# Performance work log

Hardware: AMD Instinct MI355X
Metric: run time of the kernel (lower is better)

Reference implementation:

```python
import jax, jax.numpy as jnp
import numpy as np

LN_EPS = 1e-5


def setup_inputs() -> dict:
    key = jax.random.key(0)
    ks = jax.random.split(key, 6)
    B, N, C, H = 8, 4096, 768, 12
    D = C // H
    x = jax.random.normal(ks[0], (B, N, C), dtype=jnp.float32)
    w_qkv = jax.random.normal(ks[1], (3 * C, C), dtype=jnp.float32) * (C ** -0.5)
    w_proj = jax.random.normal(ks[2], (C, C), dtype=jnp.float32) * (C ** -0.5)
    b_proj = jnp.zeros((C,), dtype=jnp.float32)
    # trunc_normal_(std=0.02) approximated by clipped normal
    p1 = jnp.clip(jax.random.normal(ks[3], (H, N), dtype=jnp.float32) * 0.02, -0.04, 0.04)
    p2 = jnp.clip(jax.random.normal(ks[4], (H, N), dtype=jnp.float32) * 0.02, -0.04, 0.04)
    gamma = jnp.ones((D,), dtype=jnp.float32)
    beta = jnp.zeros((D,), dtype=jnp.float32)
    return {"x": x, "w_qkv": w_qkv, "w_proj": w_proj, "b_proj": b_proj,
            "p1": p1, "p2": p2, "gamma": gamma, "beta": beta}


def _layernorm(h, gamma, beta):
    mu = jnp.mean(h, axis=-1, keepdims=True)
    var = jnp.var(h, axis=-1, keepdims=True)
    return (h - mu) * jax.lax.rsqrt(var + LN_EPS) * gamma + beta


def reference(x, w_qkv, w_proj, b_proj, p1, p2, gamma, beta):
    B, N, C = x.shape
    H = p1.shape[0]
    D = C // H
    # qkv projection (no bias): [B,N,3C] -> [3,B,H,N,D]
    qkv = (x @ w_qkv.T).reshape(B, N, 3, H, D).transpose(2, 0, 3, 1, 4)
    q, k, v = qkv[0], qkv[1], qkv[2]
    # weighted k*v reduction over sequence: [B,H,D]
    modulator = jnp.einsum('hn,bhnd->bhd', p2, k * v)
    modulator = _layernorm(modulator, gamma, beta)
    # broadcast modulation back over N: [B,H,N,D]
    modulator = jnp.einsum('hn,bhd->bhnd', p1, modulator)
    out = (q * modulator).transpose(0, 2, 1, 3).reshape(B, N, C)
    return out @ w_proj.T + b_proj
```

## Files before the change

kernel.cpp:

```cpp
#include <hip/hip_runtime.h>
#include <stdint.h>
#include <stddef.h>

#define LN_EPS 1e-5f

typedef __bf16 bf16;
typedef __bf16 bf16x8 __attribute__((ext_vector_type(8)));
typedef __bf16 bf16x4 __attribute__((ext_vector_type(4)));
typedef float f32x4 __attribute__((ext_vector_type(4)));

#define GL16(gp, lp)                                                                   \
  __builtin_amdgcn_global_load_lds((__attribute__((address_space(1))) uint32_t*)(gp),  \
                                   (__attribute__((address_space(3))) uint32_t*)(lp),  \
                                   16, 0, 0)

#define SBAR   asm volatile("s_barrier" ::: "memory")
#define VMW(N) asm volatile("s_waitcnt vmcnt(" #N ")" ::: "memory")
#define LGK(N) asm volatile("s_waitcnt lgkmcnt(" #N ")" ::: "memory")
#define NOWAIT ((void)0)

#define XV4   6291456
#define WQV4  442368
#define WPV4  147456
__global__ __launch_bounds__(256) void cvt_all(const float* __restrict__ x,
                                               const float* __restrict__ wq,
                                               const float* __restrict__ wp,
                                               bf16* __restrict__ xb,
                                               bf16* __restrict__ wqb,
                                               bf16* __restrict__ wpb) {
  int i = blockIdx.x * 256 + threadIdx.x;
  const float* src; bf16* dst; int off;
  if (i < XV4)              { src = x;  dst = xb;  off = i; }
  else if (i < XV4 + WQV4)  { src = wq; dst = wqb; off = i - XV4; }
  else                      { src = wp; dst = wpb; off = i - (XV4 + WQV4); }
  const float4 v = ((const float4*)src)[off];
  bf16x4 o;
  o[0] = (bf16)v.x; o[1] = (bf16)v.y; o[2] = (bf16)v.z; o[3] = (bf16)v.w;
  ((bf16x4*)dst)[off] = o;
}

#define STAGE_A2(H, SL) do {                          \
    GL16(pA0 + (H)*32, dA + (SL)*8192);               \
    GL16(pA1 + (H)*32, dA + (SL)*8192 + 4096); } while (0)

#define STAGE_B2(H, SL) do {                          \
    GL16(pB0 + (H)*32, dB + (SL)*8192);               \
    GL16(pB1 + (H)*32, dB + (SL)*8192 + 4096); } while (0)

#define RD_B(DST, SL)                                                              \
    _Pragma("unroll") for (int n = 0; n < 4; ++n)                                  \
      DST[n] = *(const bf16x8*)(ldsB + (SL)*8192 + (rB + n*16)*32 + colE)

#define RD_A0(DST, SL)                                                             \
    _Pragma("unroll") for (int m = 0; m < 4; ++m)                                  \
      DST[m] = *(const bf16x8*)(ldsA + (SL)*8192 + (rA + m*16)*32 + colE)

#define RD_A1(SL)                                                                  \
    _Pragma("unroll") for (int m = 0; m < 4; ++m)                                  \
      af1[m] = *(const bf16x8*)(ldsA + (SL)*8192 + (rA + 64 + m*16)*32 + colE)

#define MM(AF, BF, MO)                                                             \
    _Pragma("unroll") for (int m = 0; m < 4; ++m)                                  \
      _Pragma("unroll") for (int n = 0; n < 4; ++n)                                \
        acc[(MO) + m][n] = __builtin_amdgcn_mfma_f32_16x16x32_bf16(                \
            AF[m], BF[n], acc[(MO) + m][n], 0, 0, 0)

#define EV_PHASE(SL, A0C, BFC, STG, WAITV) do {       \
    RD_A1(SL);                                        \
    STG;                                              \
    LGK(4);                                           \
    __builtin_amdgcn_sched_barrier(0);                \
    __builtin_amdgcn_s_setprio(1);                    \
    MM(A0C, BFC, 0);                                  \
    __builtin_amdgcn_s_setprio(0);                    \
    WAITV;                                            \
    SBAR;                                             \
  } while (0)

#define OD_PHASE(NSL, A0N, BFN, BFC, STG, LGKW) do {  \
    RD_B(BFN, NSL);                                   \
    RD_A0(A0N, NSL);                                  \
    STG;                                              \
    LGKW;                                             \
    __builtin_amdgcn_sched_barrier(0);                \
    __builtin_amdgcn_s_setprio(1);                    \
    MM(af1, BFC, 4);                                  \
    __builtin_amdgcn_s_setprio(0);                    \
    SBAR;                                             \
  } while (0)

__device__ __forceinline__ void gemm256(const bf16* pA0, const bf16* pA1,
                                        const bf16* pB0, const bf16* pB1,
                                        bf16* sh, f32x4 acc[8][4]) {
  const int tid  = threadIdx.x;
  const int lane = tid & 63;
  const int wave = tid >> 6;
  const int wm   = wave >> 2;
  const int wn   = wave & 3;
  const int l16  = lane & 15;
  const int colE = ((((lane >> 4) * 16) ^ (((l16 >> 1) & 3) << 4)) >> 1);
  bf16* const ldsA = sh;
  bf16* const ldsB = sh + 32768;
  bf16* const dA   = ldsA + tid * 8;
  bf16* const dB   = ldsB + tid * 8;
  const int rA = wm * 128 + l16;
  const int rB = wn * 64 + l16;
  bf16x8 af0X[4], af0Y[4], af1[4], bfX[4], bfY[4];

  STAGE_A2(0, 0); STAGE_B2(0, 0);
  STAGE_A2(1, 1); STAGE_B2(1, 1);
  STAGE_A2(2, 2); STAGE_B2(2, 2);
  VMW(8);
  SBAR;
  RD_B(bfX, 0);
  RD_A0(af0X, 0);

  for (int h4 = 0; h4 < 20; h4 += 4) {
    EV_PHASE(0, af0X, bfX, STAGE_A2(h4 + 3, 3), VMW(6));
    OD_PHASE(1, af0Y, bfY, bfX, STAGE_B2(h4 + 3, 3), LGK(8));
    EV_PHASE(1, af0Y, bfY, STAGE_A2(h4 + 4, 0), VMW(6));
    OD_PHASE(2, af0X, bfX, bfY, STAGE_B2(h4 + 4, 0), LGK(8));
    EV_PHASE(2, af0X, bfX, STAGE_A2(h4 + 5, 1), VMW(6));
    OD_PHASE(3, af0Y, bfY, bfX, STAGE_B2(h4 + 5, 1), LGK(8));
    EV_PHASE(3, af0Y, bfY, STAGE_A2(h4 + 6, 2), VMW(6));
    OD_PHASE(0, af0X, bfX, bfY, STAGE_B2(h4 + 6, 2), LGK(8));
  }
  EV_PHASE(0, af0X, bfX, STAGE_A2(23, 3), VMW(6));
  OD_PHASE(1, af0Y, bfY, bfX, STAGE_B2(23, 3), LGK(8));
  EV_PHASE(1, af0Y, bfY, NOWAIT, VMW(4));
  OD_PHASE(2, af0X, bfX, bfY, NOWAIT, LGK(8));
  EV_PHASE(2, af0X, bfX, NOWAIT, VMW(0));
  OD_PHASE(3, af0Y, bfY, bfX, NOWAIT, LGK(8));
  EV_PHASE(3, af0Y, bfY, NOWAIT, NOWAIT);
  LGK(0);
  __builtin_amdgcn_sched_barrier(0);
  __builtin_amdgcn_s_setprio(1);
  MM(af1, bfY, 4);
  __builtin_amdgcn_s_setprio(0);
  asm volatile("s_waitcnt vmcnt(0) lgkmcnt(0)" ::: "memory");
  __syncthreads();
}

__global__ __launch_bounds__(512, 2) void kv_gemm_reduce(const bf16* __restrict__ A,
                                                         const bf16* __restrict__ B,
                                                         const float* __restrict__ p2,
                                                         float* __restrict__ partials) {
  __shared__ __align__(16) bf16 sh[256 * 264];
  __shared__ float red[4][2][64];

  int lin = blockIdx.y * 6 + blockIdx.x;
  lin = (lin & 7) * 96 + (lin >> 3);
  const int hh   = lin % 6;
  const int mblk = lin / 6;
  const int m0   = mblk * 256;
  const int h0   = hh * 2;

  const int tid = threadIdx.x;
  const int rr  = tid >> 2;
  const int ck  = ((tid & 3) ^ ((tid >> 3) & 3)) * 8;
  const bf16* pA0 = A + (size_t)(m0 + rr) * 768 + ck;
  const bf16* pA1 = pA0 + (size_t)128 * 768;
  const int r1 = 128 + rr;
  const int wr0 = 768 + (((rr >> 6) & 1) * 768) + (h0 + (rr >> 7)) * 64 + (rr & 63);
  const int wr1 = 768 + (((r1 >> 6) & 1) * 768) + (h0 + (r1 >> 7)) * 64 + (r1 & 63);
  const bf16* pB0 = B + (size_t)wr0 * 768 + ck;
  const bf16* pB1 = B + (size_t)wr1 * 768 + ck;

  f32x4 acc[8][4] = {};
  gemm256(pA0, pA1, pB0, pB1, sh, acc);

  const int lane = tid & 63, wave = tid >> 6;
  const int wm = wave >> 2, wn = wave & 3, l16 = lane & 15;
  const int c0 = wn * 64 + l16;
  const int r0 = wm * 128 + (lane >> 4) * 4;
#pragma unroll
  for (int ni = 0; ni < 4; ++ni)
#pragma unroll
    for (int mi = 0; mi < 8; ++mi) {
      bf16x4 pk;
      pk[0] = (bf16)acc[mi][ni][0]; pk[1] = (bf16)acc[mi][ni][1];
      pk[2] = (bf16)acc[mi][ni][2]; pk[3] = (bf16)acc[mi][ni][3];
      *(bf16x4*)(sh + (size_t)(c0 + ni * 16) * 264 + r0 + mi * 16) = pk;
    }
  __syncthreads();

  const int nq = tid >> 7, hl = (tid >> 6) & 1, d = tid & 63;
  const float* pw = p2 + (size_t)(h0 + hl) * 4096 + (m0 & 4095) + nq * 64;
  const bf16* pk = sh + (size_t)(hl * 128 + d) * 264 + nq * 64;
  const bf16* pv = sh + (size_t)(hl * 128 + 64 + d) * 264 + nq * 64;
  float s = 0.f;
#pragma unroll
  for (int nb = 0; nb < 8; ++nb) {
    const bf16x8 k8 = *(const bf16x8*)(pk + nb * 8);
    const bf16x8 v8 = *(const bf16x8*)(pv + nb * 8);
#pragma unroll
    for (int e = 0; e < 8; ++e)
      s += pw[nb * 8 + e] * (float)k8[e] * (float)v8[e];
  }
  red[nq][hl][d] = s;
  __syncthreads();
  if (tid < 128) {
    const int hx = tid >> 6, dd = tid & 63;
    partials[((size_t)mblk * 12 + h0 + hx) * 64 + dd] =
        red[0][hx][dd] + red[1][hx][dd] + red[2][hx][dd] + red[3][hx][dd];
  }
}

__global__ __launch_bounds__(64) void mod_reduce_ln(const float* __restrict__ partials,
                                                    const float* __restrict__ gamma,
                                                    const float* __restrict__ beta,
                                                    float* __restrict__ mod) {
  const int h = blockIdx.x, b = blockIdx.y;
  const int d = threadIdx.x;

  const float* p = partials + ((size_t)(b * 16) * 12 + h) * 64 + d;
  float s = 0.f;
#pragma unroll
  for (int mb = 0; mb < 16; ++mb) s += p[(size_t)mb * 12 * 64];

  float sum = s, sumsq = s * s;
#pragma unroll
  for (int o = 32; o > 0; o >>= 1) {
    sum   += __shfl_xor(sum, o);
    sumsq += __shfl_xor(sumsq, o);
  }
  const float mu  = sum * (1.f / 64.f);
  const float var = sumsq * (1.f / 64.f) - mu * mu;
  const float r   = rsqrtf(var + LN_EPS);
  mod[(b * 12 + h) * 64 + d] = (s - mu) * r * gamma[d] + beta[d];
}

__global__ __launch_bounds__(512, 2) void q_gemm_mod(const bf16* __restrict__ A,
                                                     const bf16* __restrict__ B,
                                                     const float* __restrict__ p1,
                                                     const float* __restrict__ mod,
                                                     bf16* __restrict__ amod) {
  __shared__ __align__(16) bf16 sh[65536];

  int lin = blockIdx.y * 3 + blockIdx.x;
  lin = (lin & 7) * 48 + (lin >> 3);
  const int n0 = (lin % 3) * 256;
  const int m0 = (lin / 3) * 256;

  const int tid = threadIdx.x;
  const int rr  = tid >> 2;
  const int ck  = ((tid & 3) ^ ((tid >> 3) & 3)) * 8;
  const bf16* pA0 = A + (size_t)(m0 + rr) * 768 + ck;
  const bf16* pA1 = pA0 + (size_t)128 * 768;
  const bf16* pB0 = B + (size_t)(n0 + rr) * 768 + ck;
  const bf16* pB1 = pB0 + (size_t)128 * 768;

  f32x4 acc[8][4] = {};
  gemm256(pA0, pA1, pB0, pB1, sh, acc);

  const int lane = tid & 63, wave = tid >> 6;
  const int wm = wave >> 2, wn = wave & 3, l16 = lane & 15;
  const int row0 = m0 + wm * 128 + (lane >> 4) * 4;
  const int col0 = n0 + wn * 64 + l16;
  const int b    = m0 >> 12;
  const int h    = (n0 >> 6) + wn;

  float p1v[8][4];
#pragma unroll
  for (int mi = 0; mi < 8; ++mi)
#pragma unroll
    for (int r = 0; r < 4; ++r)
      p1v[mi][r] = p1[(size_t)h * 4096 + ((row0 + mi * 16 + r) & 4095)];
  float mv[4];
#pragma unroll
  for (int ni = 0; ni < 4; ++ni) mv[ni] = mod[b * 768 + col0 + ni * 16];

#pragma unroll
  for (int mi = 0; mi < 8; ++mi)
#pragma unroll
    for (int ni = 0; ni < 4; ++ni)
#pragma unroll
      for (int r = 0; r < 4; ++r)
        amod[(size_t)(row0 + mi * 16 + r) * 768 + col0 + ni * 16] =
            (bf16)(acc[mi][ni][r] * p1v[mi][r] * mv[ni]);
}

__global__ __launch_bounds__(512, 2) void gemm_proj(const bf16* __restrict__ A,
                                                    const bf16* __restrict__ B,
                                                    const float* __restrict__ bias,
                                                    float* __restrict__ C) {
  __shared__ __align__(16) bf16 sh[65536];

  int lin = blockIdx.y * 3 + blockIdx.x;
  lin = (lin & 7) * 48 + (lin >> 3);
  const int n0 = (lin % 3) * 256;
  const int m0 = (lin / 3) * 256;

  const int tid = threadIdx.x;
  const int rr  = tid >> 2;
  const int ck  = ((tid & 3) ^ ((tid >> 3) & 3)) * 8;
  const bf16* pA0 = A + (size_t)(m0 + rr) * 768 + ck;
  const bf16* pA1 = pA0 + (size_t)128 * 768;
  const bf16* pB0 = B + (size_t)(n0 + rr) * 768 + ck;
  const bf16* pB1 = pB0 + (size_t)128 * 768;

  f32x4 acc[8][4] = {};
  gemm256(pA0, pA1, pB0, pB1, sh, acc);

  const int lane = tid & 63, wave = tid >> 6;
  const int wm = wave >> 2, wn = wave & 3, l16 = lane & 15;
  const int row0 = m0 + wm * 128 + (lane >> 4) * 4;
  const int col0 = n0 + wn * 64 + l16;
#pragma unroll
  for (int ni = 0; ni < 4; ++ni) {
    const int col = col0 + ni * 16;
    const float bv = bias[col];
#pragma unroll
    for (int mi = 0; mi < 8; ++mi)
#pragma unroll
      for (int r = 0; r < 4; ++r)
        C[(size_t)(row0 + mi * 16 + r) * 768 + col] = acc[mi][ni][r] + bv;
  }
}

extern "C" void kernel_launch(void* const* d_in, const int* in_sizes, int n_in,
                              void* d_out, int out_size, void* d_ws, size_t ws_size,
                              hipStream_t stream) {
  (void)in_sizes; (void)n_in; (void)out_size; (void)ws_size;

  const float* x      = (const float*)d_in[0];
  const float* w_qkv  = (const float*)d_in[1];
  const float* w_proj = (const float*)d_in[2];
  const float* b_proj = (const float*)d_in[3];
  const float* p1     = (const float*)d_in[4];
  const float* p2     = (const float*)d_in[5];
  const float* gamma  = (const float*)d_in[6];
  const float* beta   = (const float*)d_in[7];
  float* out = (float*)d_out;

  char* ws = (char*)d_ws;
  bf16*  xb       = (bf16*)(ws + 0);
  bf16*  wqb      = (bf16*)(ws + 50331648);
  bf16*  wpb      = (bf16*)(ws + 53870592);
  bf16*  amod     = (bf16*)(ws + 55050240);
  float* partials = (float*)(ws + 105381888);
  float* mod      = (float*)(ws + 106168320);

  cvt_all<<<26880, 256, 0, stream>>>(x, w_qkv, w_proj, xb, wqb, wpb);

  kv_gemm_reduce<<<dim3(6, 128), 512, 0, stream>>>(xb, wqb, p2, partials);

  mod_reduce_ln<<<dim3(12, 8), 64, 0, stream>>>(partials, gamma, beta, mod);

  q_gemm_mod<<<dim3(3, 128), 512, 0, stream>>>(xb, wqb, p1, mod, amod);

  gemm_proj<<<dim3(3, 128), 512, 0, stream>>>(amod, wpb, b_proj, out);
}
```

Before: 374.5 us.

## Specialize loader waves per operand with deeper A prefetch and swizzled reduction LDS

The shared GEMM core now splits the load work: waves 0-3 load only A tiles through a 6-slot ring five stages ahead, and waves 4-7 load only B tiles through a 3-slot ring two stages ahead. This replaces the uniform 4-slot ring where every thread staged both operands. Block-to-tile mapping is changed to an XCD-aware order. The kv reduction epilogue adds an XOR swizzle to its LDS transpose and reads p2 as float4. LDS per block grows, which may affect occupancy at two blocks per CU, and the per-wave wait counts diverge, making the barrier schedule more fragile.

```diff
diff --git a/kernel.cpp b/kernel.cpp
--- a/kernel.cpp
+++ b/kernel.cpp
@@ -39,25 +39,24 @@
   ((bf16x4*)dst)[off] = o;
 }
 
-#define STAGE_A2(H, SL) do {                          \
-    GL16(pA0 + (H)*32, dA + (SL)*8192);               \
-    GL16(pA1 + (H)*32, dA + (SL)*8192 + 4096); } while (0)
-
-#define STAGE_B2(H, SL) do {                          \
-    GL16(pB0 + (H)*32, dB + (SL)*8192);               \
-    GL16(pB1 + (H)*32, dB + (SL)*8192 + 4096); } while (0)
+#define STG(KH, SL) do {                                         \
+    GL16(g0 + (size_t)(KH) * 32, myLds + (SL) * 8192);           \
+    GL16(g1 + (size_t)(KH) * 32, myLds + (SL) * 8192 + 512);     \
+    GL16(g2 + (size_t)(KH) * 32, myLds + (SL) * 8192 + 1024);    \
+    GL16(g3 + (size_t)(KH) * 32, myLds + (SL) * 8192 + 1536);    \
+  } while (0)
 
 #define RD_B(DST, SL)                                                              \
     _Pragma("unroll") for (int n = 0; n < 4; ++n)                                  \
-      DST[n] = *(const bf16x8*)(ldsB + (SL)*8192 + (rB + n*16)*32 + colE)
+      DST[n] = *(const bf16x8*)(ldsB + (SL) * 8192 + (rB + n * 16) * 32 + colE)
 
 #define RD_A0(DST, SL)                                                             \
     _Pragma("unroll") for (int m = 0; m < 4; ++m)                                  \
-      DST[m] = *(const bf16x8*)(ldsA + (SL)*8192 + (rA + m*16)*32 + colE)
+      DST[m] = *(const bf16x8*)(ldsA + (SL) * 8192 + (rA + m * 16) * 32 + colE)
 
 #define RD_A1(SL)                                                                  \
     _Pragma("unroll") for (int m = 0; m < 4; ++m)                                  \
-      af1[m] = *(const bf16x8*)(ldsA + (SL)*8192 + (rA + 64 + m*16)*32 + colE)
+      af1[m] = *(const bf16x8*)(ldsA + (SL) * 8192 + (rA + 64 + m * 16) * 32 + colE)
 
 #define MM(AF, BF, MO)                                                             \
     _Pragma("unroll") for (int m = 0; m < 4; ++m)                                  \
@@ -65,23 +64,23 @@
         acc[(MO) + m][n] = __builtin_amdgcn_mfma_f32_16x16x32_bf16(                \
             AF[m], BF[n], acc[(MO) + m][n], 0, 0, 0)
 
-#define EV_PHASE(SL, A0C, BFC, STG, WAITV) do {       \
-    RD_A1(SL);                                        \
-    STG;                                              \
+#define EVP(KH, A0C, BFC, STGA, WA, WB) do {          \
+    RD_A1((KH) % 6);                                  \
+    if ((STGA) && isA) STG((KH) + 5, ((KH) + 5) % 6); \
     LGK(4);                                           \
     __builtin_amdgcn_sched_barrier(0);                \
     __builtin_amdgcn_s_setprio(1);                    \
     MM(A0C, BFC, 0);                                  \
     __builtin_amdgcn_s_setprio(0);                    \
-    WAITV;                                            \
+    if (isA) { WA; } else { WB; }                     \
     SBAR;                                             \
   } while (0)
 
-#define OD_PHASE(NSL, A0N, BFN, BFC, STG, LGKW) do {  \
-    RD_B(BFN, NSL);                                   \
-    RD_A0(A0N, NSL);                                  \
-    STG;                                              \
-    LGKW;                                             \
+#define ODP(KH, A0N, BFN, BFC, STGB) do {             \
+    RD_B(BFN, ((KH) + 1) % 3);                        \
+    RD_A0(A0N, ((KH) + 1) % 6);                       \
+    if ((STGB) && !isA) STG((KH) + 2, ((KH) + 2) % 3);\
+    LGK(8);                                           \
     __builtin_amdgcn_sched_barrier(0);                \
     __builtin_amdgcn_s_setprio(1);                    \
     MM(af1, BFC, 4);                                  \
@@ -89,49 +88,50 @@
     SBAR;                                             \
   } while (0)
 
-__device__ __forceinline__ void gemm256(const bf16* pA0, const bf16* pA1,
-                                        const bf16* pB0, const bf16* pB1,
-                                        bf16* sh, f32x4 acc[8][4]) {
+#define KHPAIR(KA, KB)                                            \
+  EVP(KA, af0X, bfX, 1, VMW(16), VMW(0)); ODP(KA, af0Y, bfY, bfX, 1); \
+  EVP(KB, af0Y, bfY, 1, VMW(16), VMW(0)); ODP(KB, af0X, bfX, bfY, 1);
+
+__device__ __forceinline__ void gemm256(const bf16* gsrc, bf16* sh, f32x4 acc[8][4]) {
   const int tid  = threadIdx.x;
   const int lane = tid & 63;
   const int wave = tid >> 6;
-  const int wm   = wave >> 2;
-  const int wn   = wave & 3;
+  const bool isA = wave < 4;
+  const int grp_w = wave & 3;
   const int l16  = lane & 15;
   const int colE = ((((lane >> 4) * 16) ^ (((l16 >> 1) & 3) << 4)) >> 1);
-  bf16* const ldsA = sh;
-  bf16* const ldsB = sh + 32768;
-  bf16* const dA   = ldsA + tid * 8;
-  bf16* const dB   = ldsB + tid * 8;
+  bf16* const ldsA  = sh;
+  bf16* const ldsB  = sh + 49152;
+  bf16* const myLds = (isA ? ldsA : ldsB) + grp_w * 2048 + lane * 8;
+  const bf16* g0 = gsrc;
+  const bf16* g1 = gsrc + 12288;
+  const bf16* g2 = gsrc + 24576;
+  const bf16* g3 = gsrc + 36864;
+  const int wm = wave >> 2, wn = wave & 3;
   const int rA = wm * 128 + l16;
   const int rB = wn * 64 + l16;
   bf16x8 af0X[4], af0Y[4], af1[4], bfX[4], bfY[4];
 
-  STAGE_A2(0, 0); STAGE_B2(0, 0);
-  STAGE_A2(1, 1); STAGE_B2(1, 1);
-  STAGE_A2(2, 2); STAGE_B2(2, 2);
-  VMW(8);
+  if (isA) {
+    STG(0, 0); STG(1, 1); STG(2, 2); STG(3, 3); STG(4, 4);
+    VMW(16);
+  } else {
+    STG(0, 0); STG(1, 1);
+    VMW(4);
+  }
   SBAR;
   RD_B(bfX, 0);
   RD_A0(af0X, 0);
 
-  for (int h4 = 0; h4 < 20; h4 += 4) {
-    EV_PHASE(0, af0X, bfX, STAGE_A2(h4 + 3, 3), VMW(6));
-    OD_PHASE(1, af0Y, bfY, bfX, STAGE_B2(h4 + 3, 3), LGK(8));
-    EV_PHASE(1, af0Y, bfY, STAGE_A2(h4 + 4, 0), VMW(6));
-    OD_PHASE(2, af0X, bfX, bfY, STAGE_B2(h4 + 4, 0), LGK(8));
-    EV_PHASE(2, af0X, bfX, STAGE_A2(h4 + 5, 1), VMW(6));
-    OD_PHASE(3, af0Y, bfY, bfX, STAGE_B2(h4 + 5, 1), LGK(8));
-    EV_PHASE(3, af0Y, bfY, STAGE_A2(h4 + 6, 2), VMW(6));
-    OD_PHASE(0, af0X, bfX, bfY, STAGE_B2(h4 + 6, 2), LGK(8));
-  }
-  EV_PHASE(0, af0X, bfX, STAGE_A2(23, 3), VMW(6));
-  OD_PHASE(1, af0Y, bfY, bfX, STAGE_B2(23, 3), LGK(8));
-  EV_PHASE(1, af0Y, bfY, NOWAIT, VMW(4));
-  OD_PHASE(2, af0X, bfX, bfY, NOWAIT, LGK(8));
-  EV_PHASE(2, af0X, bfX, NOWAIT, VMW(0));
-  OD_PHASE(3, af0Y, bfY, bfX, NOWAIT, LGK(8));
-  EV_PHASE(3, af0Y, bfY, NOWAIT, NOWAIT);
+  KHPAIR(0, 1)  KHPAIR(2, 3)  KHPAIR(4, 5)  KHPAIR(6, 7)  KHPAIR(8, 9)
+  KHPAIR(10, 11)  KHPAIR(12, 13)  KHPAIR(14, 15)  KHPAIR(16, 17)
+
+  EVP(18, af0X, bfX, 1, VMW(16), VMW(0)); ODP(18, af0Y, bfY, bfX, 1);
+  EVP(19, af0Y, bfY, 0, VMW(12), VMW(0)); ODP(19, af0X, bfX, bfY, 1);
+  EVP(20, af0X, bfX, 0, VMW(8),  VMW(0)); ODP(20, af0Y, bfY, bfX, 1);
+  EVP(21, af0Y, bfY, 0, VMW(4),  VMW(0)); ODP(21, af0X, bfX, bfY, 1);
+  EVP(22, af0X, bfX, 0, VMW(0),  VMW(0)); ODP(22, af0Y, bfY, bfX, 0);
+  EVP(23, af0Y, bfY, 0, NOWAIT, NOWAIT);
   LGK(0);
   __builtin_amdgcn_sched_barrier(0);
   __builtin_amdgcn_s_setprio(1);
@@ -145,57 +145,69 @@
                                                          const bf16* __restrict__ B,
                                                          const float* __restrict__ p2,
                                                          float* __restrict__ partials) {
-  __shared__ __align__(16) bf16 sh[256 * 264];
+  __shared__ __align__(16) bf16 sh[73728];
   __shared__ float red[4][2][64];
 
-  int lin = blockIdx.y * 6 + blockIdx.x;
-  lin = (lin & 7) * 96 + (lin >> 3);
-  const int hh   = lin % 6;
-  const int mblk = lin / 6;
+  const int lin  = blockIdx.y * 6 + blockIdx.x;
+  const int xcd  = lin & 7;
+  const int j    = lin >> 3;
+  const int hh   = j % 6;
+  const int mblk = xcd + 8 * (j / 6);
   const int m0   = mblk * 256;
   const int h0   = hh * 2;
 
-  const int tid = threadIdx.x;
-  const int rr  = tid >> 2;
-  const int ck  = ((tid & 3) ^ ((tid >> 3) & 3)) * 8;
-  const bf16* pA0 = A + (size_t)(m0 + rr) * 768 + ck;
-  const bf16* pA1 = pA0 + (size_t)128 * 768;
-  const int r1 = 128 + rr;
-  const int wr0 = 768 + (((rr >> 6) & 1) * 768) + (h0 + (rr >> 7)) * 64 + (rr & 63);
-  const int wr1 = 768 + (((r1 >> 6) & 1) * 768) + (h0 + (r1 >> 7)) * 64 + (r1 & 63);
-  const bf16* pB0 = B + (size_t)wr0 * 768 + ck;
-  const bf16* pB1 = B + (size_t)wr1 * 768 + ck;
+  const int tid = threadIdx.x, lane = tid & 63, wave = tid >> 6;
+  const int ck = ((lane & 3) ^ ((lane >> 3) & 3)) * 8;
+  const bf16* gsrc;
+  if (wave < 4) {
+    gsrc = A + (size_t)(m0 + wave * 64 + (lane >> 2)) * 768 + ck;
+  } else {
+    const int w1 = wave - 4;
+    const int wrow = 768 + (w1 & 1) * 768 + (h0 + (w1 >> 1)) * 64 + (lane >> 2);
+    gsrc = B + (size_t)wrow * 768 + ck;
+  }
 
   f32x4 acc[8][4] = {};
-  gemm256(pA0, pA1, pB0, pB1, sh, acc);
-
-  const int lane = tid & 63, wave = tid >> 6;
+  gemm256(gsrc, sh, acc);
+
   const int wm = wave >> 2, wn = wave & 3, l16 = lane & 15;
   const int c0 = wn * 64 + l16;
   const int r0 = wm * 128 + (lane >> 4) * 4;
 #pragma unroll
-  for (int ni = 0; ni < 4; ++ni)
+  for (int ni = 0; ni < 4; ++ni) {
+    const int c   = c0 + ni * 16;
+    const int key = (c ^ (c >> 3)) & 7;
 #pragma unroll
     for (int mi = 0; mi < 8; ++mi) {
+      const int r = r0 + mi * 16;
       bf16x4 pk;
       pk[0] = (bf16)acc[mi][ni][0]; pk[1] = (bf16)acc[mi][ni][1];
       pk[2] = (bf16)acc[mi][ni][2]; pk[3] = (bf16)acc[mi][ni][3];
-      *(bf16x4*)(sh + (size_t)(c0 + ni * 16) * 264 + r0 + mi * 16) = pk;
+      *(bf16x4*)(sh + (size_t)c * 264 + (((r >> 3) ^ key) << 3) + (r & 7)) = pk;
     }
+  }
   __syncthreads();
 
   const int nq = tid >> 7, hl = (tid >> 6) & 1, d = tid & 63;
-  const float* pw = p2 + (size_t)(h0 + hl) * 4096 + (m0 & 4095) + nq * 64;
-  const bf16* pk = sh + (size_t)(hl * 128 + d) * 264 + nq * 64;
-  const bf16* pv = sh + (size_t)(hl * 128 + 64 + d) * 264 + nq * 64;
+  const float4* pw4 = (const float4*)(p2 + (size_t)(h0 + hl) * 4096 + (m0 & 4095) + nq * 64);
+  const int ck_  = hl * 128 + d;
+  const int cv_  = ck_ + 64;
+  const int keyk = (ck_ ^ (ck_ >> 3)) & 7;
+  const int keyv = (cv_ ^ (cv_ >> 3)) & 7;
+  const bf16* bk = sh + (size_t)ck_ * 264;
+  const bf16* bv = sh + (size_t)cv_ * 264;
   float s = 0.f;
 #pragma unroll
   for (int nb = 0; nb < 8; ++nb) {
-    const bf16x8 k8 = *(const bf16x8*)(pk + nb * 8);
-    const bf16x8 v8 = *(const bf16x8*)(pv + nb * 8);
-#pragma unroll
-    for (int e = 0; e < 8; ++e)
-      s += pw[nb * 8 + e] * (float)k8[e] * (float)v8[e];
+    const int blk = nq * 8 + nb;
+    const bf16x8 k8 = *(const bf16x8*)(bk + ((blk ^ keyk) << 3));
+    const bf16x8 v8 = *(const bf16x8*)(bv + ((blk ^ keyv) << 3));
+    const float4 w0 = pw4[nb * 2];
+    const float4 w1 = pw4[nb * 2 + 1];
+    s += w0.x * (float)k8[0] * (float)v8[0] + w0.y * (float)k8[1] * (float)v8[1]
+       + w0.z * (float)k8[2] * (float)v8[2] + w0.w * (float)k8[3] * (float)v8[3]
+       + w1.x * (float)k8[4] * (float)v8[4] + w1.y * (float)k8[5] * (float)v8[5]
+       + w1.z * (float)k8[6] * (float)v8[6] + w1.w * (float)k8[7] * (float)v8[7];
   }
   red[nq][hl][d] = s;
   __syncthreads();
@@ -235,25 +247,25 @@
                                                      const float* __restrict__ p1,
                                                      const float* __restrict__ mod,
                                                      bf16* __restrict__ amod) {
-  __shared__ __align__(16) bf16 sh[65536];
-
-  int lin = blockIdx.y * 3 + blockIdx.x;
-  lin = (lin & 7) * 48 + (lin >> 3);
-  const int n0 = (lin % 3) * 256;
-  const int m0 = (lin / 3) * 256;
-
-  const int tid = threadIdx.x;
-  const int rr  = tid >> 2;
-  const int ck  = ((tid & 3) ^ ((tid >> 3) & 3)) * 8;
-  const bf16* pA0 = A + (size_t)(m0 + rr) * 768 + ck;
-  const bf16* pA1 = pA0 + (size_t)128 * 768;
-  const bf16* pB0 = B + (size_t)(n0 + rr) * 768 + ck;
-  const bf16* pB1 = pB0 + (size_t)128 * 768;
+  __shared__ __align__(16) bf16 sh[73728];
+
+  const int lin  = blockIdx.y * 3 + blockIdx.x;
+  const int xcd  = lin & 7;
+  const int j    = lin >> 3;
+  const int nblk = j % 3;
+  const int mblk = xcd + 8 * (j / 3);
+  const int n0   = nblk * 256;
+  const int m0   = mblk * 256;
+
+  const int tid = threadIdx.x, lane = tid & 63, wave = tid >> 6;
+  const int ck = ((lane & 3) ^ ((lane >> 3) & 3)) * 8;
+  const bf16* gsrc;
+  if (wave < 4) gsrc = A + (size_t)(m0 + wave * 64 + (lane >> 2)) * 768 + ck;
+  else          gsrc = B + (size_t)(n0 + (wave - 4) * 64 + (lane >> 2)) * 768 + ck;
 
   f32x4 acc[8][4] = {};
-  gemm256(pA0, pA1, pB0, pB1, sh, acc);
-
-  const int lane = tid & 63, wave = tid >> 6;
+  gemm256(gsrc, sh, acc);
+
   const int wm = wave >> 2, wn = wave & 3, l16 = lane & 15;
   const int row0 = m0 + wm * 128 + (lane >> 4) * 4;
   const int col0 = n0 + wn * 64 + l16;
@@ -284,25 +296,25 @@
                                                     const bf16* __restrict__ B,
                                                     const float* __restrict__ bias,
                                                     float* __restrict__ C) {
-  __shared__ __align__(16) bf16 sh[65536];
-
-  int lin = blockIdx.y * 3 + blockIdx.x;
-  lin = (lin & 7) * 48 + (lin >> 3);
-  const int n0 = (lin % 3) * 256;
-  const int m0 = (lin / 3) * 256;
-
-  const int tid = threadIdx.x;
-  const int rr  = tid >> 2;
-  const int ck  = ((tid & 3) ^ ((tid >> 3) & 3)) * 8;
-  const bf16* pA0 = A + (size_t)(m0 + rr) * 768 + ck;
-  const bf16* pA1 = pA0 + (size_t)128 * 768;
-  const bf16* pB0 = B + (size_t)(n0 + rr) * 768 + ck;
-  const bf16* pB1 = pB0 + (size_t)128 * 768;
+  __shared__ __align__(16) bf16 sh[73728];
+
+  const int lin  = blockIdx.y * 3 + blockIdx.x;
+  const int xcd  = lin & 7;
+  const int j    = lin >> 3;
+  const int nblk = j % 3;
+  const int mblk = xcd + 8 * (j / 3);
+  const int n0   = nblk * 256;
+  const int m0   = mblk * 256;
+
+  const int tid = threadIdx.x, lane = tid & 63, wave = tid >> 6;
+  const int ck = ((lane & 3) ^ ((lane >> 3) & 3)) * 8;
+  const bf16* gsrc;
+  if (wave < 4) gsrc = A + (size_t)(m0 + wave * 64 + (lane >> 2)) * 768 + ck;
+  else          gsrc = B + (size_t)(n0 + (wave - 4) * 64 + (lane >> 2)) * 768 + ck;
 
   f32x4 acc[8][4] = {};
-  gemm256(pA0, pA1, pB0, pB1, sh, acc);
-
-  const int lane = tid & 63, wave = tid >> 6;
+  gemm256(gsrc, sh, acc);
+
   const int wm = wave >> 2, wn = wave & 3, l16 = lane & 15;
   const int row0 = m0 + wm * 128 + (lane >> 4) * 4;
   const int col0 = n0 + wn * 64 + l16;
```

New measurement: 389.5 us. +4.0%, slower.
